# Kernel optimization log

Hardware: AMD Instinct MI355X
Metric: run time of the kernel (lower is better)

Reference implementation:

```python
import jax, jax.numpy as jnp
import numpy as np

B, N, C, H, W = 32, 32, 3, 32, 32
HID, OUT = 256, 128


def _conv(x, w, b):
    y = jax.lax.conv_general_dilated(
        x, w, window_strides=(1, 1), padding="SAME",
        dimension_numbers=("NCHW", "OIHW", "NCHW"))
    return y + b[None, :, None, None]


def _sage(h, lw, lb, rw):
    # PyG SAGEConv with mean aggregation on a fully-connected graph (no self-loops):
    # agg_i = (sum_j h_j - h_i) / (N-1); out = agg @ lw.T + lb + h @ rw.T
    n = h.shape[1]
    agg = (jnp.sum(h, axis=1, keepdims=True) - h) / (n - 1)
    return jnp.einsum('bnd,od->bno', agg, lw) + lb + jnp.einsum('bnd,od->bno', h, rw)


def setup_inputs() -> dict:
    key = jax.random.key(0)
    ks = jax.random.split(key, 16)
    def g(k, shape, scale):
        return jax.random.normal(k, shape, dtype=jnp.float32) * scale
    return {
        "x": jax.random.normal(ks[0], (B, N, C, H, W), dtype=jnp.float32),
        "mask": jnp.ones((B, N), dtype=jnp.float32),
        "conv1_w": g(ks[1], (64, C, 3, 3), 0.1),
        "conv1_b": jnp.zeros((64,), jnp.float32),
        "conv2_w": g(ks[2], (128, 64, 3, 3), 0.05),
        "conv2_b": jnp.zeros((128,), jnp.float32),
        "fc_w": g(ks[3], (HID, 128), 0.08),
        "fc_b": jnp.zeros((HID,), jnp.float32),
        "s1_lw": g(ks[4], (HID, HID), 0.06),
        "s1_lb": jnp.zeros((HID,), jnp.float32),
        "s1_rw": g(ks[5], (HID, HID), 0.06),
        "s2_lw": g(ks[6], (OUT, HID), 0.06),
        "s2_lb": jnp.zeros((OUT,), jnp.float32),
        "s2_rw": g(ks[7], (OUT, HID), 0.06),
    }


def reference(x, mask, conv1_w, conv1_b, conv2_w, conv2_b, fc_w, fc_b,
              s1_lw, s1_lb, s1_rw, s2_lw, s2_lb, s2_rw):
    b, n, c, h, w = x.shape
    z = x.reshape(b * n, c, h, w)
    z = jax.nn.relu(_conv(z, conv1_w, conv1_b))
    z = jax.nn.relu(_conv(z, conv2_w, conv2_b))
    z = jnp.mean(z, axis=(2, 3))                      # AdaptiveAvgPool2d((1,1)) + flatten
    z = z @ fc_w.T + fc_b                             # [B*N, HID]
    z = z.reshape(b, n, -1) * mask[:, :, None]
    z = jax.nn.relu(_sage(z, s1_lw, s1_lb, s1_rw))
    z = _sage(z, s2_lw, s2_lb, s2_rw)                 # [B, N, OUT]
    return z
```

## Files before the change

kernel.cpp:

```cpp
#include <hip/hip_runtime.h>
#include <hip/hip_bf16.h>


typedef __attribute__((ext_vector_type(8))) short bfrag;
typedef __attribute__((ext_vector_type(4))) float f32x4;
typedef __attribute__((ext_vector_type(16))) float f32x16;

static __device__ __forceinline__ unsigned short f2bf(float f) {
    union { float f; unsigned u; } v; v.f = f;
    unsigned r = v.u + 0x7fff + ((v.u >> 16) & 1);
    return (unsigned short)(r >> 16);
}

static __device__ __forceinline__ unsigned cvtpk(float lo, float hi) {
    unsigned r;
    asm("v_cvt_pk_bf16_f32 %0, %1, %2" : "=v"(r) : "v"(lo), "v"(hi));
    return r;
}

static __device__ __forceinline__ void gl_lds16(const short* g, short* l) {
    __builtin_amdgcn_global_load_lds(
        (const __attribute__((address_space(1))) unsigned int*)g,
        (__attribute__((address_space(3))) unsigned int*)l, 16, 0, 0);
}

__global__ __launch_bounds__(256) void prep_kernel(
    const float* __restrict__ s1lw, const float* __restrict__ s1rw,
    const float* __restrict__ s2lw, const float* __restrict__ s2rw,
    const float* __restrict__ c2w, const float* __restrict__ c1w,
    const float* __restrict__ c1b, const float* __restrict__ fcw,
    float* __restrict__ l1T, float* __restrict__ w1pT,
    float* __restrict__ l2T, float* __restrict__ w2pT,
    float* __restrict__ fwT,
    short* __restrict__ w2c, short* __restrict__ w1b) {
    int i = blockIdx.x * 256 + threadIdx.x;
    const float inv31 = 1.f / 31.f;
    if (i < 65536) {
        int d = i >> 8, o = i & 255;
        float lw = s1lw[o * 256 + d];
        l1T[i]  = lw;
        w1pT[i] = s1rw[o * 256 + d] - lw * inv31;
    }
    if (i < 32768) {
        int d = i >> 7, o = i & 127;
        float lw = s2lw[o * 256 + d];
        l2T[i]  = lw;
        w2pT[i] = s2rw[o * 256 + d] - lw * inv31;
        int c = i >> 8, o2 = i & 255;
        fwT[i] = fcw[o2 * 128 + c];
    }
    if (i < 73728) {
        int tap = i >> 13, r = i & 8191;
        int ks = r >> 11, hi = (r >> 10) & 1, oc = (r >> 3) & 127, j = i & 7;
        int ic = ks * 16 + hi * 8 + j;
        w2c[i] = (short)f2bf(c2w[(oc * 64 + ic) * 9 + tap]);
    }
    if (i < 2048) {
        int oc = i >> 5, k = i & 31;
        float v = (k < 27) ? c1w[oc * 27 + k] : (k == 27 ? c1b[oc] : 0.f);
        w1b[i] = (short)f2bf(v);
    }
}

__global__ __launch_bounds__(256, 2) void fused_conv_kernel(
    const float* __restrict__ x, const short* __restrict__ w1b,
    const short* __restrict__ w2c, const float* __restrict__ b2,
    float* __restrict__ pooled4) {
    const int band = blockIdx.x, img = blockIdx.y;
    __shared__ short xt[3 * 12 * 34];
    __shared__ short c1t[10 * 34 * 72];
    __shared__ short bufB[3][4096];
    __shared__ float wsum[4][128];
    const int t = threadIdx.x;
    const int w = t >> 6, lane = t & 63;
    const int ln15 = lane & 15, q8 = (lane >> 4) * 8;
    const int ln31 = lane & 31, hi = lane >> 5;

    const float* xi = x + img * 3072;
    for (int idx = t; idx < 1224; idx += 256) {
        int c = idx / 408, rem = idx % 408, r = rem / 34, col = rem % 34;
        int y = band * 8 - 2 + r, xx = col - 1;
        float v = 0.f;
        if ((unsigned)y < 32u && (unsigned)xx < 32u) v = xi[c * 1024 + y * 32 + xx];
        xt[idx] = (short)f2bf(v);
    }
    {
        f32x4 z = {0.f, 0.f, 0.f, 0.f};
        for (int i = t; i < 180; i += 256) {
            int r = i / 18, rem = i % 18, side = rem / 9, q = rem % 9;
            *(f32x4*)(c1t + (r * 34 + side * 33) * 72 + q * 8) = z;
        }
    }
    bfrag b1f[4];
#pragma unroll
    for (int ot = 0; ot < 4; ++ot)
        b1f[ot] = *(const bfrag*)(w1b + (ot * 16 + ln15) * 32 + q8);

    int xOff[8]; int kMask[8]; int kOvr[8];
#pragma unroll
    for (int j = 0; j < 8; ++j) {
        int k = q8 + j;
        int c = (k * 57) >> 9;
        int rem = k - 9 * c;
        int dy = (rem * 11) >> 5;
        int dx = rem - 3 * dy;
        int cc = c < 3 ? c : 2;
        xOff[j] = cc * 408 + dy * 34 + dx;
        kMask[j] = (c < 3) ? 0xFFFF : 0;
        kOvr[j]  = (c < 3) ? 0 : (k == 27 ? 0x3F80 : 0);
    }
    __syncthreads();

    {
        const short* src = w2c + t * 8;
        short* dst = (short*)bufB + t * 8;
        gl_lds16(src, dst);
        gl_lds16(src + 2048, dst + 2048);
        gl_lds16(src + 4096, dst + 4096);
        gl_lds16(src + 6144, dst + 6144);
    }

#pragma unroll 1
    for (int pt = 0; pt < 5; ++pt) {
        const int tile = w * 5 + pt;
        const int r = tile >> 1, xcb = (tile & 1) << 4;
        const int baseA = r * 34 + xcb + ln15;
        bfrag a1f;
#pragma unroll
        for (int j = 0; j < 8; ++j)
            a1f[j] = (short)((xt[xOff[j] + baseA] & kMask[j]) | kOvr[j]);
        f32x4 acc1[4];
#pragma unroll
        for (int ot = 0; ot < 4; ++ot) {
#pragma unroll
            for (int rg = 0; rg < 4; ++rg) acc1[ot][rg] = 0.f;
            acc1[ot] = __builtin_amdgcn_mfma_f32_16x16x32_bf16(
                b1f[ot], a1f, acc1[ot], 0, 0, 0);
        }
        const int y = band * 8 - 1 + r;
        const bool valid = (unsigned)y < 32u;
        const int waddr = (r * 34 + xcb + ln15 + 1) * 72 + (lane >> 4) * 4;
#pragma unroll
        for (int ot = 0; ot < 4; ++ot) {
            uint2 pk = {0u, 0u};
            if (valid) {
                pk.x = cvtpk(fmaxf(acc1[ot][0], 0.f), fmaxf(acc1[ot][1], 0.f));
                pk.y = cvtpk(fmaxf(acc1[ot][2], 0.f), fmaxf(acc1[ot][3], 0.f));
            }
            *(uint2*)&c1t[waddr + ot * 16] = pk;
        }
    }
    __syncthreads();

    float b2v[4];
#pragma unroll
    for (int ot = 0; ot < 4; ++ot) b2v[ot] = b2[ot * 32 + ln31];

    f32x16 acc[2][4];
#pragma unroll
    for (int pt = 0; pt < 2; ++pt)
#pragma unroll
        for (int ot = 0; ot < 4; ++ot)
#pragma unroll
            for (int rg = 0; rg < 16; ++rg) acc[pt][ot][rg] = 0.f;

    const int aB0 = (w * 2 * 34 + ln31) * 72 + hi * 8;
    const int aB1 = aB0 + 34 * 72;
    const int bOff = hi * 1024 + ln31 * 8;
    const short* stSrc = w2c + t * 8;
    short* stDst = (short*)bufB + t * 8;

    auto stage = [&](int st) {
        const short* src = stSrc + st * 4096;
        short* dst = stDst + (st % 3) * 4096;
        gl_lds16(src, dst);
        gl_lds16(src + 2048, dst + 2048);
    };
    auto prefB = [&](bfrag* bf, int st) {
        const short* bc = (const short*)bufB + (st % 3) * 4096 + bOff;
#pragma unroll
        for (int kk = 0; kk < 2; ++kk)
#pragma unroll
            for (int ot = 0; ot < 4; ++ot)
                bf[kk * 4 + ot] = *(const bfrag*)(bc + kk * 2048 + ot * 256);
    };
    auto body = [&](int st, const bfrag* bCur, bfrag* bNext) {
        if (st + 2 < 18) stage(st + 2);
        const int tap = st >> 1, kh = st & 1;
        const int dy = (tap * 11) >> 5, dx = tap - 3 * dy;
        const int aOff = (dy * 34 + dx) * 72 + kh * 32;
        bfrag af0 = *(const bfrag*)&c1t[aB0 + aOff];
        bfrag af1 = *(const bfrag*)&c1t[aB0 + aOff + 16];
        bfrag af2 = *(const bfrag*)&c1t[aB1 + aOff];
        bfrag af3 = *(const bfrag*)&c1t[aB1 + aOff + 16];
        if (st + 1 < 18) prefB(bNext, st + 1);
        __builtin_amdgcn_s_setprio(1);
#pragma unroll
        for (int ot = 0; ot < 4; ++ot)
            acc[0][ot] = __builtin_amdgcn_mfma_f32_32x32x16_bf16(
                af0, bCur[ot], acc[0][ot], 0, 0, 0);
#pragma unroll
        for (int ot = 0; ot < 4; ++ot)
            acc[0][ot] = __builtin_amdgcn_mfma_f32_32x32x16_bf16(
                af1, bCur[4 + ot], acc[0][ot], 0, 0, 0);
#pragma unroll
        for (int ot = 0; ot < 4; ++ot)
            acc[1][ot] = __builtin_amdgcn_mfma_f32_32x32x16_bf16(
                af2, bCur[ot], acc[1][ot], 0, 0, 0);
#pragma unroll
        for (int ot = 0; ot < 4; ++ot)
            acc[1][ot] = __builtin_amdgcn_mfma_f32_32x32x16_bf16(
                af3, bCur[4 + ot], acc[1][ot], 0, 0, 0);
        __builtin_amdgcn_s_setprio(0);
        asm volatile("s_waitcnt vmcnt(0)" ::: "memory");
        __builtin_amdgcn_s_barrier();
    };

    bfrag bX[8], bY[8];
    prefB(bX, 0);
#pragma unroll 1
    for (int st = 0; st < 18; st += 2) {
        body(st, bX, bY);
        body(st + 1, bY, bX);
    }

#pragma unroll
    for (int ot = 0; ot < 4; ++ot) {
        float s = 0.f;
#pragma unroll
        for (int pt = 0; pt < 2; ++pt)
#pragma unroll
            for (int rg = 0; rg < 16; ++rg)
                s += fmaxf(acc[pt][ot][rg] + b2v[ot], 0.f);
        s += __shfl_xor(s, 32, 64);
        if (lane < 32) wsum[w][ot * 32 + ln31] = s;
    }
    __syncthreads();
    if (t < 128) {
        pooled4[((size_t)img * 4 + band) * 128 + t] =
            wsum[0][t] + wsum[1][t] + wsum[2][t] + wsum[3][t];
    }
}

__global__ __launch_bounds__(256) void fc_kernel(
    const float* __restrict__ pooled4, const float* __restrict__ fwT,
    const float* __restrict__ fb, const float* __restrict__ mask,
    float* __restrict__ z1) {
    const int img = blockIdx.x;
    __shared__ float m[128];
    const int t = threadIdx.x;
    if (t < 128) {
        const float* p = pooled4 + (size_t)img * 4 * 128 + t;
        m[t] = (p[0] + p[128] + p[256] + p[384]) * (1.f / 1024.f);
    }
    __syncthreads();
    float acc = fb[t];
#pragma unroll 4
    for (int c = 0; c < 128; ++c) acc = fmaf(m[c], fwT[c * 256 + t], acc);
    z1[img * 256 + t] = acc * mask[img];
}

__global__ __launch_bounds__(256) void sage1_kernel(
    const float* __restrict__ z1, const float* __restrict__ l1T,
    const float* __restrict__ lb, const float* __restrict__ w1pT,
    float* __restrict__ z2) {
    const int bx = blockIdx.x;
    const int bb = bx >> 4, chunk = (bx >> 1) & 7, ohalf = bx & 1;
    __shared__ float h[32 * 256];
    __shared__ float sl[256];
    __shared__ float part[2][128];
    __shared__ float pacc[2][4][128];
    const int t = threadIdx.x;
    const int oo = t & 127, dh = t >> 7;
    const int o = ohalf * 128 + oo;
    const float* zb = z1 + bb * 8192;
    for (int idx = t; idx < 8192; idx += 256) h[idx] = zb[idx];
    __syncthreads();
    {
        float s = 0.f;
#pragma unroll
        for (int n = 0; n < 32; ++n) s += h[n * 256 + t];
        sl[t] = s * (1.f / 31.f);
    }
    __syncthreads();
    const int d0b = dh * 128;
    float c = 0.f;
#pragma unroll 4
    for (int d = 0; d < 128; ++d) c = fmaf(sl[d0b + d], l1T[(d0b + d) * 256 + o], c);
    part[dh][oo] = c;
    float acc[4] = {0.f, 0.f, 0.f, 0.f};
    for (int d = 0; d < 128; d += 4) {
        float wv0 = w1pT[(d0b + d + 0) * 256 + o];
        float wv1 = w1pT[(d0b + d + 1) * 256 + o];
        float wv2 = w1pT[(d0b + d + 2) * 256 + o];
        float wv3 = w1pT[(d0b + d + 3) * 256 + o];
#pragma unroll
        for (int i = 0; i < 4; ++i) {
            f32x4 hv = *(const f32x4*)&h[(chunk * 4 + i) * 256 + d0b + d];
            acc[i] = fmaf(hv[0], wv0, acc[i]);
            acc[i] = fmaf(hv[1], wv1, acc[i]);
            acc[i] = fmaf(hv[2], wv2, acc[i]);
            acc[i] = fmaf(hv[3], wv3, acc[i]);
        }
    }
#pragma unroll
    for (int i = 0; i < 4; ++i) pacc[dh][i][oo] = acc[i];
    __syncthreads();
    const float cf = part[0][oo] + part[1][oo] + lb[o];
#pragma unroll
    for (int ii = 0; ii < 2; ++ii) {
        const int i = dh * 2 + ii;
        float v = cf + pacc[0][i][oo] + pacc[1][i][oo];
        z2[(bb * 32 + chunk * 4 + i) * 256 + o] = fmaxf(v, 0.f);
    }
}

__global__ __launch_bounds__(256) void sage2_kernel(
    const float* __restrict__ z2, const float* __restrict__ l2T,
    const float* __restrict__ lb, const float* __restrict__ w2pT,
    float* __restrict__ out) {
    const int bx = blockIdx.x;
    const int bb = bx >> 4, chunk = bx & 15;
    __shared__ float h[32 * 256];
    __shared__ float sl[256];
    __shared__ float part[2][128];
    __shared__ float pacc[2][2][128];
    const int t = threadIdx.x;
    const int oo = t & 127, dh = t >> 7;
    const float* zb = z2 + bb * 8192;
    for (int idx = t; idx < 8192; idx += 256) h[idx] = zb[idx];
    __syncthreads();
    {
        float s = 0.f;
#pragma unroll
        for (int n = 0; n < 32; ++n) s += h[n * 256 + t];
        sl[t] = s * (1.f / 31.f);
    }
    __syncthreads();
    const int d0b = dh * 128;
    const int n0 = chunk * 2;
    float c = 0.f;
#pragma unroll 4
    for (int d = 0; d < 128; ++d) c = fmaf(sl[d0b + d], l2T[(d0b + d) * 128 + oo], c);
    part[dh][oo] = c;
    float acc[2] = {0.f, 0.f};
    for (int d = 0; d < 128; d += 4) {
        float wv0 = w2pT[(d0b + d + 0) * 128 + oo];
        float wv1 = w2pT[(d0b + d + 1) * 128 + oo];
        float wv2 = w2pT[(d0b + d + 2) * 128 + oo];
        float wv3 = w2pT[(d0b + d + 3) * 128 + oo];
#pragma unroll
        for (int i = 0; i < 2; ++i) {
            f32x4 hv = *(const f32x4*)&h[(n0 + i) * 256 + d0b + d];
            acc[i] = fmaf(hv[0], wv0, acc[i]);
            acc[i] = fmaf(hv[1], wv1, acc[i]);
            acc[i] = fmaf(hv[2], wv2, acc[i]);
            acc[i] = fmaf(hv[3], wv3, acc[i]);
        }
    }
#pragma unroll
    for (int i = 0; i < 2; ++i) pacc[dh][i][oo] = acc[i];
    __syncthreads();
    const float cf = part[0][oo] + part[1][oo] + lb[oo];
    {
        const int i = dh;
        float v = cf + pacc[0][i][oo] + pacc[1][i][oo];
        out[(size_t)(bb * 32 + n0 + i) * 128 + oo] = v;
    }
}

extern "C" void kernel_launch(void* const* d_in, const int* in_sizes, int n_in,
                              void* d_out, int out_size, void* d_ws, size_t ws_size,
                              hipStream_t stream) {
    const float* x    = (const float*)d_in[0];
    const float* mask = (const float*)d_in[1];
    const float* c1w  = (const float*)d_in[2];
    const float* c1b  = (const float*)d_in[3];
    const float* c2w  = (const float*)d_in[4];
    const float* c2b  = (const float*)d_in[5];
    const float* fcw  = (const float*)d_in[6];
    const float* fcb  = (const float*)d_in[7];
    const float* s1lw = (const float*)d_in[8];
    const float* s1lb = (const float*)d_in[9];
    const float* s1rw = (const float*)d_in[10];
    const float* s2lw = (const float*)d_in[11];
    const float* s2lb = (const float*)d_in[12];
    const float* s2rw = (const float*)d_in[13];
    float* out = (float*)d_out;

    char* ws = (char*)d_ws;
    float* pooled4 = (float*)(ws);
    float* z1      = (float*)(ws + 2048u * 1024);
    float* z2      = (float*)(ws + 3072u * 1024);
    float* l1T     = (float*)(ws + 4096u * 1024);
    float* w1pT    = (float*)(ws + 4352u * 1024);
    float* l2T     = (float*)(ws + 4608u * 1024);
    float* w2pT    = (float*)(ws + 4736u * 1024);
    float* fwT     = (float*)(ws + 4864u * 1024);
    short* w2c     = (short*)(ws + 4992u * 1024);
    short* w1b     = (short*)(ws + 5136u * 1024);

    prep_kernel<<<dim3(288), 256, 0, stream>>>(s1lw, s1rw, s2lw, s2rw, c2w, c1w, c1b,
                                               fcw, l1T, w1pT, l2T, w2pT, fwT, w2c, w1b);
    fused_conv_kernel<<<dim3(4, 1024), 256, 0, stream>>>(x, w1b, w2c, c2b, pooled4);
    fc_kernel<<<dim3(1024), 256, 0, stream>>>(pooled4, fwT, fcb, mask, z1);
    sage1_kernel<<<dim3(512), 256, 0, stream>>>(z1, l1T, s1lb, w1pT, z2);
    sage2_kernel<<<dim3(512), 256, 0, stream>>>(z2, l2T, s2lb, w2pT, out);
}
```

Measured before the change: 258.9 us.

## Split conv2 output channels across 8 waves and load weights directly from global

The fused conv kernel moves from 4 to 8 waves per block. Each pair of waves shares a row tile and splits the 128 output channels in half, which lowers accumulator register pressure and allows higher occupancy. The triple-buffered LDS staging of conv2 weights and its per-step barriers are removed, and B fragments are now read straight from global/L2 each step. The prep kernel is rewritten to read weights coalesced and scatter-write the transposed layouts. The trade-off is exposed global-load latency inside the MFMA loop and duplicate A-fragment LDS reads across the channel halves.

```diff
diff --git a/kernel.cpp b/kernel.cpp
--- a/kernel.cpp
+++ b/kernel.cpp
@@ -16,12 +16,6 @@
     unsigned r;
     asm("v_cvt_pk_bf16_f32 %0, %1, %2" : "=v"(r) : "v"(lo), "v"(hi));
     return r;
-}
-
-static __device__ __forceinline__ void gl_lds16(const short* g, short* l) {
-    __builtin_amdgcn_global_load_lds(
-        (const __attribute__((address_space(1))) unsigned int*)g,
-        (__attribute__((address_space(3))) unsigned int*)l, 16, 0, 0);
 }
 
 __global__ __launch_bounds__(256) void prep_kernel(
@@ -36,24 +30,27 @@
     int i = blockIdx.x * 256 + threadIdx.x;
     const float inv31 = 1.f / 31.f;
     if (i < 65536) {
-        int d = i >> 8, o = i & 255;
-        float lw = s1lw[o * 256 + d];
-        l1T[i]  = lw;
-        w1pT[i] = s1rw[o * 256 + d] - lw * inv31;
+        int o = i >> 8, d = i & 255;
+        float lw = s1lw[i];
+        float rw = s1rw[i];
+        l1T[d * 256 + o]  = lw;
+        w1pT[d * 256 + o] = rw - lw * inv31;
     }
     if (i < 32768) {
-        int d = i >> 7, o = i & 127;
-        float lw = s2lw[o * 256 + d];
-        l2T[i]  = lw;
-        w2pT[i] = s2rw[o * 256 + d] - lw * inv31;
-        int c = i >> 8, o2 = i & 255;
-        fwT[i] = fcw[o2 * 128 + c];
+        int o = i >> 8, d = i & 255;
+        float lw = s2lw[i];
+        float rw = s2rw[i];
+        l2T[d * 128 + o]  = lw;
+        w2pT[d * 128 + o] = rw - lw * inv31;
+        int o2 = i >> 7, c = i & 127;
+        fwT[c * 256 + o2] = fcw[i];
     }
     if (i < 73728) {
-        int tap = i >> 13, r = i & 8191;
-        int ks = r >> 11, hi = (r >> 10) & 1, oc = (r >> 3) & 127, j = i & 7;
-        int ic = ks * 16 + hi * 8 + j;
-        w2c[i] = (short)f2bf(c2w[(oc * 64 + ic) * 9 + tap]);
+        int oc = i / 576, rem = i - oc * 576;
+        int ic = rem / 9, tap = rem - ic * 9;
+        int widx = tap * 8192 + (ic >> 4) * 2048 + ((ic >> 3) & 1) * 1024
+                 + oc * 8 + (ic & 7);
+        w2c[widx] = (short)f2bf(c2w[i]);
     }
     if (i < 2048) {
         int oc = i >> 5, k = i & 31;
@@ -62,22 +59,22 @@
     }
 }
 
-__global__ __launch_bounds__(256, 2) void fused_conv_kernel(
+__global__ __launch_bounds__(512, 4) void fused_conv_kernel(
     const float* __restrict__ x, const short* __restrict__ w1b,
     const short* __restrict__ w2c, const float* __restrict__ b2,
     float* __restrict__ pooled4) {
     const int band = blockIdx.x, img = blockIdx.y;
-    __shared__ short xt[3 * 12 * 34];
     __shared__ short c1t[10 * 34 * 72];
-    __shared__ short bufB[3][4096];
-    __shared__ float wsum[4][128];
+    __shared__ float xw[612];
+    short* xt = (short*)xw;
     const int t = threadIdx.x;
     const int w = t >> 6, lane = t & 63;
     const int ln15 = lane & 15, q8 = (lane >> 4) * 8;
     const int ln31 = lane & 31, hi = lane >> 5;
+    const int wq = w & 3, oh = w >> 2;
 
     const float* xi = x + img * 3072;
-    for (int idx = t; idx < 1224; idx += 256) {
+    for (int idx = t; idx < 1224; idx += 512) {
         int c = idx / 408, rem = idx % 408, r = rem / 34, col = rem % 34;
         int y = band * 8 - 2 + r, xx = col - 1;
         float v = 0.f;
@@ -86,15 +83,15 @@
     }
     {
         f32x4 z = {0.f, 0.f, 0.f, 0.f};
-        for (int i = t; i < 180; i += 256) {
+        for (int i = t; i < 180; i += 512) {
             int r = i / 18, rem = i % 18, side = rem / 9, q = rem % 9;
             *(f32x4*)(c1t + (r * 34 + side * 33) * 72 + q * 8) = z;
         }
     }
-    bfrag b1f[4];
-#pragma unroll
-    for (int ot = 0; ot < 4; ++ot)
-        b1f[ot] = *(const bfrag*)(w1b + (ot * 16 + ln15) * 32 + q8);
+    bfrag b1f[2];
+#pragma unroll
+    for (int ot = 0; ot < 2; ++ot)
+        b1f[ot] = *(const bfrag*)(w1b + ((oh * 2 + ot) * 16 + ln15) * 32 + q8);
 
     int xOff[8]; int kMask[8]; int kOvr[8];
 #pragma unroll
@@ -111,27 +108,18 @@
     }
     __syncthreads();
 
-    {
-        const short* src = w2c + t * 8;
-        short* dst = (short*)bufB + t * 8;
-        gl_lds16(src, dst);
-        gl_lds16(src + 2048, dst + 2048);
-        gl_lds16(src + 4096, dst + 4096);
-        gl_lds16(src + 6144, dst + 6144);
-    }
-
 #pragma unroll 1
     for (int pt = 0; pt < 5; ++pt) {
-        const int tile = w * 5 + pt;
+        const int tile = wq * 5 + pt;
         const int r = tile >> 1, xcb = (tile & 1) << 4;
         const int baseA = r * 34 + xcb + ln15;
         bfrag a1f;
 #pragma unroll
         for (int j = 0; j < 8; ++j)
             a1f[j] = (short)((xt[xOff[j] + baseA] & kMask[j]) | kOvr[j]);
-        f32x4 acc1[4];
-#pragma unroll
-        for (int ot = 0; ot < 4; ++ot) {
+        f32x4 acc1[2];
+#pragma unroll
+        for (int ot = 0; ot < 2; ++ot) {
 #pragma unroll
             for (int rg = 0; rg < 4; ++rg) acc1[ot][rg] = 0.f;
             acc1[ot] = __builtin_amdgcn_mfma_f32_16x16x32_bf16(
@@ -141,51 +129,40 @@
         const bool valid = (unsigned)y < 32u;
         const int waddr = (r * 34 + xcb + ln15 + 1) * 72 + (lane >> 4) * 4;
 #pragma unroll
-        for (int ot = 0; ot < 4; ++ot) {
+        for (int ot = 0; ot < 2; ++ot) {
             uint2 pk = {0u, 0u};
             if (valid) {
                 pk.x = cvtpk(fmaxf(acc1[ot][0], 0.f), fmaxf(acc1[ot][1], 0.f));
                 pk.y = cvtpk(fmaxf(acc1[ot][2], 0.f), fmaxf(acc1[ot][3], 0.f));
             }
-            *(uint2*)&c1t[waddr + ot * 16] = pk;
-        }
-    }
-    __syncthreads();
-
-    float b2v[4];
-#pragma unroll
-    for (int ot = 0; ot < 4; ++ot) b2v[ot] = b2[ot * 32 + ln31];
-
-    f32x16 acc[2][4];
+            *(uint2*)&c1t[waddr + (oh * 2 + ot) * 16] = pk;
+        }
+    }
+    __syncthreads();
+
+    float b2v[2];
+#pragma unroll
+    for (int ot = 0; ot < 2; ++ot) b2v[ot] = b2[oh * 64 + ot * 32 + ln31];
+
+    f32x16 acc[2][2];
 #pragma unroll
     for (int pt = 0; pt < 2; ++pt)
 #pragma unroll
-        for (int ot = 0; ot < 4; ++ot)
+        for (int ot = 0; ot < 2; ++ot)
 #pragma unroll
             for (int rg = 0; rg < 16; ++rg) acc[pt][ot][rg] = 0.f;
 
-    const int aB0 = (w * 2 * 34 + ln31) * 72 + hi * 8;
+    const int aB0 = (wq * 2 * 34 + ln31) * 72 + hi * 8;
     const int aB1 = aB0 + 34 * 72;
-    const int bOff = hi * 1024 + ln31 * 8;
-    const short* stSrc = w2c + t * 8;
-    short* stDst = (short*)bufB + t * 8;
-
-    auto stage = [&](int st) {
-        const short* src = stSrc + st * 4096;
-        short* dst = stDst + (st % 3) * 4096;
-        gl_lds16(src, dst);
-        gl_lds16(src + 2048, dst + 2048);
-    };
-    auto prefB = [&](bfrag* bf, int st) {
-        const short* bc = (const short*)bufB + (st % 3) * 4096 + bOff;
-#pragma unroll
-        for (int kk = 0; kk < 2; ++kk)
-#pragma unroll
-            for (int ot = 0; ot < 4; ++ot)
-                bf[kk * 4 + ot] = *(const bfrag*)(bc + kk * 2048 + ot * 256);
-    };
-    auto body = [&](int st, const bfrag* bCur, bfrag* bNext) {
-        if (st + 2 < 18) stage(st + 2);
+    const short* bBase = w2c + hi * 1024 + oh * 512 + ln31 * 8;
+
+#pragma unroll 1
+    for (int st = 0; st < 18; ++st) {
+        const short* p = bBase + st * 4096;
+        bfrag bg00 = *(const bfrag*)(p);
+        bfrag bg01 = *(const bfrag*)(p + 256);
+        bfrag bg10 = *(const bfrag*)(p + 2048);
+        bfrag bg11 = *(const bfrag*)(p + 2304);
         const int tap = st >> 1, kh = st & 1;
         const int dy = (tap * 11) >> 5, dx = tap - 3 * dy;
         const int aOff = (dy * 34 + dx) * 72 + kh * 32;
@@ -193,39 +170,21 @@
         bfrag af1 = *(const bfrag*)&c1t[aB0 + aOff + 16];
         bfrag af2 = *(const bfrag*)&c1t[aB1 + aOff];
         bfrag af3 = *(const bfrag*)&c1t[aB1 + aOff + 16];
-        if (st + 1 < 18) prefB(bNext, st + 1);
         __builtin_amdgcn_s_setprio(1);
-#pragma unroll
-        for (int ot = 0; ot < 4; ++ot)
-            acc[0][ot] = __builtin_amdgcn_mfma_f32_32x32x16_bf16(
-                af0, bCur[ot], acc[0][ot], 0, 0, 0);
-#pragma unroll
-        for (int ot = 0; ot < 4; ++ot)
-            acc[0][ot] = __builtin_amdgcn_mfma_f32_32x32x16_bf16(
-                af1, bCur[4 + ot], acc[0][ot], 0, 0, 0);
-#pragma unroll
-        for (int ot = 0; ot < 4; ++ot)
-            acc[1][ot] = __builtin_amdgcn_mfma_f32_32x32x16_bf16(
-                af2, bCur[ot], acc[1][ot], 0, 0, 0);
-#pragma unroll
-        for (int ot = 0; ot < 4; ++ot)
-            acc[1][ot] = __builtin_amdgcn_mfma_f32_32x32x16_bf16(
-                af3, bCur[4 + ot], acc[1][ot], 0, 0, 0);
+        acc[0][0] = __builtin_amdgcn_mfma_f32_32x32x16_bf16(af0, bg00, acc[0][0], 0, 0, 0);
+        acc[0][1] = __builtin_amdgcn_mfma_f32_32x32x16_bf16(af0, bg01, acc[0][1], 0, 0, 0);
+        acc[1][0] = __builtin_amdgcn_mfma_f32_32x32x16_bf16(af2, bg00, acc[1][0], 0, 0, 0);
+        acc[1][1] = __builtin_amdgcn_mfma_f32_32x32x16_bf16(af2, bg01, acc[1][1], 0, 0, 0);
+        acc[0][0] = __builtin_amdgcn_mfma_f32_32x32x16_bf16(af1, bg10, acc[0][0], 0, 0, 0);
+        acc[0][1] = __builtin_amdgcn_mfma_f32_32x32x16_bf16(af1, bg11, acc[0][1], 0, 0, 0);
+        acc[1][0] = __builtin_amdgcn_mfma_f32_32x32x16_bf16(af3, bg10, acc[1][0], 0, 0, 0);
+        acc[1][1] = __builtin_amdgcn_mfma_f32_32x32x16_bf16(af3, bg11, acc[1][1], 0, 0, 0);
         __builtin_amdgcn_s_setprio(0);
-        asm volatile("s_waitcnt vmcnt(0)" ::: "memory");
-        __builtin_amdgcn_s_barrier();
-    };
-
-    bfrag bX[8], bY[8];
-    prefB(bX, 0);
-#pragma unroll 1
-    for (int st = 0; st < 18; st += 2) {
-        body(st, bX, bY);
-        body(st + 1, bY, bX);
-    }
-
-#pragma unroll
-    for (int ot = 0; ot < 4; ++ot) {
+    }
+
+    float* wsum = xw;
+#pragma unroll
+    for (int ot = 0; ot < 2; ++ot) {
         float s = 0.f;
 #pragma unroll
         for (int pt = 0; pt < 2; ++pt)
@@ -233,12 +192,14 @@
             for (int rg = 0; rg < 16; ++rg)
                 s += fmaxf(acc[pt][ot][rg] + b2v[ot], 0.f);
         s += __shfl_xor(s, 32, 64);
-        if (lane < 32) wsum[w][ot * 32 + ln31] = s;
+        if (lane < 32) wsum[(wq * 2 + oh) * 64 + ot * 32 + ln31] = s;
     }
     __syncthreads();
     if (t < 128) {
+        const int ohh = t >> 6, ww = t & 63;
         pooled4[((size_t)img * 4 + band) * 128 + t] =
-            wsum[0][t] + wsum[1][t] + wsum[2][t] + wsum[3][t];
+            wsum[(0 * 2 + ohh) * 64 + ww] + wsum[(1 * 2 + ohh) * 64 + ww] +
+            wsum[(2 * 2 + ohh) * 64 + ww] + wsum[(3 * 2 + ohh) * 64 + ww];
     }
 }
 
@@ -402,7 +363,7 @@
 
     prep_kernel<<<dim3(288), 256, 0, stream>>>(s1lw, s1rw, s2lw, s2rw, c2w, c1w, c1b,
                                                fcw, l1T, w1pT, l2T, w2pT, fwT, w2c, w1b);
-    fused_conv_kernel<<<dim3(4, 1024), 256, 0, stream>>>(x, w1b, w2c, c2b, pooled4);
+    fused_conv_kernel<<<dim3(4, 1024), 512, 0, stream>>>(x, w1b, w2c, c2b, pooled4);
     fc_kernel<<<dim3(1024), 256, 0, stream>>>(pooled4, fwT, fcb, mask, z1);
     sage1_kernel<<<dim3(512), 256, 0, stream>>>(z1, l1T, s1lb, w1pT, z2);
     sage2_kernel<<<dim3(512), 256, 0, stream>>>(z2, l2T, s2lb, w2pT, out);
```

Measured after the change: 276.4 us. +6.8%, slower.
